# Kernel optimization log

Hardware: AMD Instinct MI355X
Metric: run time of the kernel (lower is better)

## Reference

```python
import jax, jax.numpy as jnp
import numpy as np

DIM = 256
HEADS = 8
G = 8            # group (window) size per axis
POS_DIM = 16     # (dim // 4) // 4
MLP_HIDDEN = 4 * DIM


def layernorm(x, g, b, eps=1e-5):
    m = x.mean(-1, keepdims=True)
    v = ((x - m) ** 2).mean(-1, keepdims=True)
    return (x - m) / jnp.sqrt(v + eps) * g + b


def setup_inputs() -> dict:
    key = jax.random.key(0)
    ks = jax.random.split(key, 32)
    s = 0.02
    d = {}
    d['x'] = jax.random.normal(ks[0], (1, 32768, DIM), jnp.float32)
    d['y'] = jax.random.normal(ks[1], (1, 32768, DIM), jnp.float32)
    d['n1_g'] = jnp.ones((DIM,), jnp.float32)
    d['n1_b'] = jnp.zeros((DIM,), jnp.float32)
    d['qkv_w'] = jax.random.normal(ks[2], (DIM, 3 * DIM), jnp.float32) * s
    d['qkv_b'] = jnp.zeros((3 * DIM,), jnp.float32)
    d['pp_w'] = jax.random.normal(ks[3], (3, POS_DIM), jnp.float32) * s
    d['pp_b'] = jnp.zeros((POS_DIM,), jnp.float32)
    d['p1_lng'] = jnp.ones((POS_DIM,), jnp.float32)
    d['p1_lnb'] = jnp.zeros((POS_DIM,), jnp.float32)
    d['p1_w'] = jax.random.normal(ks[4], (POS_DIM, POS_DIM), jnp.float32) * s
    d['p1_b'] = jnp.zeros((POS_DIM,), jnp.float32)
    d['p2_lng'] = jnp.ones((POS_DIM,), jnp.float32)
    d['p2_lnb'] = jnp.zeros((POS_DIM,), jnp.float32)
    d['p2_w'] = jax.random.normal(ks[5], (POS_DIM, POS_DIM), jnp.float32) * s
    d['p2_b'] = jnp.zeros((POS_DIM,), jnp.float32)
    d['p3_lng'] = jnp.ones((POS_DIM,), jnp.float32)
    d['p3_lnb'] = jnp.zeros((POS_DIM,), jnp.float32)
    d['p3_w'] = jax.random.normal(ks[6], (POS_DIM, HEADS), jnp.float32) * s
    d['p3_b'] = jnp.zeros((HEADS,), jnp.float32)
    d['proj_w'] = jax.random.normal(ks[7], (DIM, DIM), jnp.float32) * s
    d['proj_b'] = jnp.zeros((DIM,), jnp.float32)
    d['n2_g'] = jnp.ones((DIM,), jnp.float32)
    d['n2_b'] = jnp.zeros((DIM,), jnp.float32)
    d['fc1_w'] = jax.random.normal(ks[8], (DIM, MLP_HIDDEN), jnp.float32) * s
    d['fc1_b'] = jnp.zeros((MLP_HIDDEN,), jnp.float32)
    d['fc2_w'] = jax.random.normal(ks[9], (MLP_HIDDEN, DIM), jnp.float32) * s
    d['fc2_b'] = jnp.zeros((DIM,), jnp.float32)
    d['H'] = 32
    d['W'] = 32
    d['D'] = 32
    return d


def reference(x, y, n1_g, n1_b, qkv_w, qkv_b, pp_w, pp_b,
              p1_lng, p1_lnb, p1_w, p1_b, p2_lng, p2_lnb, p2_w, p2_b,
              p3_lng, p3_lnb, p3_w, p3_b, proj_w, proj_b,
              n2_g, n2_b, fc1_w, fc1_b, fc2_w, fc2_b, H, W, D):
    B, L, C = x.shape
    nh, g = HEADS, G
    hd = C // nh
    shortcut = x
    xn = layernorm(x, n1_g, n1_b)
    xv = xn.reshape(B, H, W, D, C)
    yv = y.reshape(B, H, W, D, C)  # note: y is NOT normed in the original

    # SDA window partition (H,W,D divisible by g -> no padding, zero mask)
    def part(t):
        t = t.reshape(B, H // g, g, W // g, g, D // g, g, C)
        t = t.transpose(0, 1, 3, 5, 2, 4, 6, 7)
        return t.reshape(-1, g * g * g, C)

    xg, yg = part(xv), part(yv)
    B_, N, _ = xg.shape

    # original quirk: self.qkv used for BOTH x and y (qkv_y layer unused)
    qkv = (xg @ qkv_w + qkv_b).reshape(B_, N, 3, nh, hd).transpose(2, 0, 3, 1, 4)
    qkv_y = (yg @ qkv_w + qkv_b).reshape(B_, N, 3, nh, hd).transpose(2, 0, 3, 1, 4)
    q = qkv[0] * (hd ** -0.5)
    k_y, v_y = qkv_y[1], qkv_y[2]

    attn = jnp.einsum('bhnd,bhmd->bhnm', q, k_y)  # [B_, nh, N, N]

    # dynamic relative position bias (small MLP + gather)
    rng = jnp.arange(1 - g, g)
    bh, bw, bd = jnp.meshgrid(rng, rng, rng, indexing='ij')
    biases = jnp.stack([bh, bw, bd], -1).reshape(-1, 3).astype(x.dtype)  # [(2g-1)^3, 3]
    pos = biases @ pp_w + pp_b
    pos = jax.nn.relu(layernorm(pos, p1_lng, p1_lnb)) @ p1_w + p1_b
    pos = jax.nn.relu(layernorm(pos, p2_lng, p2_lnb)) @ p2_w + p2_b
    pos = jax.nn.relu(layernorm(pos, p3_lng, p3_lnb)) @ p3_w + p3_b  # [(2g-1)^3, nh]

    c = jnp.arange(g)
    ch, cw, cd = jnp.meshgrid(c, c, c, indexing='ij')
    cf = jnp.stack([ch, cw, cd], 0).reshape(3, -1)          # [3, g^3]
    rel = (cf[:, :, None] - cf[:, None, :]).transpose(1, 2, 0) + (g - 1)
    idx = rel[..., 0] * (2 * g - 1) * (2 * g - 1) + rel[..., 1] * (2 * g - 1) + rel[..., 2]
    bias = pos[idx].transpose(2, 0, 1)  # [nh, N, N]

    attn = jax.nn.softmax(attn + bias[None], axis=-1)
    out = jnp.einsum('bhnm,bhmd->bhnd', attn, v_y).transpose(0, 2, 1, 3).reshape(B_, N, C)
    out = out @ proj_w + proj_b

    # reverse window partition
    out = out.reshape(B, H // g, W // g, D // g, g, g, g, C)
    out = out.transpose(0, 1, 4, 2, 5, 3, 6, 7).reshape(B, H * W * D, C)

    x = shortcut + out
    x2 = layernorm(x, n2_g, n2_b)
    h = jax.nn.gelu(x2 @ fc1_w + fc1_b, approximate=False)
    x = x + (h @ fc2_w + fc2_b)
    return x
```

## Files before the change

kernel.cpp:

```cpp
#include <hip/hip_runtime.h>
#include <cstdint>
#include <cstddef>

typedef unsigned int u32;
typedef unsigned short u16;
typedef __attribute__((ext_vector_type(8))) short bf16x8;
typedef __attribute__((ext_vector_type(4))) float f32x4;

#define DEV __device__ __forceinline__

DEV float b2f(u16 u){ return __uint_as_float(((u32)u)<<16); }
DEV u16 f2b(float f){ u32 x = __float_as_uint(f); x += 0x7fffu + ((x>>16)&1u); return (u16)(x>>16); }
DEV u32 pk2(float a, float b){
  u32 r;
  asm("v_cvt_pk_bf16_f32 %0, %1, %2" : "=v"(r) : "v"(a), "v"(b));
  return r;
}

DEV void gll16(const void* g, void* l){
  __builtin_amdgcn_global_load_lds((const __attribute__((address_space(1))) u32*)g,
                                   (__attribute__((address_space(3))) u32*)l, 16, 0, 0);
}

DEV void win_n(int r, int& win, int& n){
  int d_ = r & 31, w_ = (r>>5)&31, h_ = r>>10;
  win = ((h_>>3)<<4) | ((w_>>3)<<2) | (d_>>3);
  n   = ((h_&7)<<6)  | ((w_&7)<<3)  | (d_&7);
}
DEV int tok_of(int r){
  int win = r>>9, nn = r&511;
  int bh = win>>4, bw=(win>>2)&3, bd=win&3;
  int ih = nn>>6,  iw=(nn>>3)&7,  id=nn&7;
  return ((bh*8+ih)<<10) | ((bw*8+iw)<<5) | (bd*8+id);
}


__global__ void wtrall_k(const float* __restrict__ qkv_w, const float* __restrict__ proj_w,
                         const float* __restrict__ fc1_w, const float* __restrict__ fc2_w,
                         u16* __restrict__ qkvT, u16* __restrict__ projT,
                         u16* __restrict__ fc1T, u16* __restrict__ fc2T){
  int f = blockIdx.x*256 + threadIdx.x;
  const float* w; u16* wt; int g; bool k10 = false; int N;
  if (f < 196608)      { w=qkv_w;  wt=qkvT;  g=f;        N=768;  }
  else if (f < 262144) { w=proj_w; wt=projT; g=f-196608; N=256;  }
  else if (f < 524288) { w=fc1_w;  wt=fc1T;  g=f-262144; N=1024; }
  else                 { w=fc2_w;  wt=fc2T;  g=f-524288; N=256;  k10=true; }
  int n = k10 ? (g>>10) : (g>>8);
  int k = k10 ? (g&1023) : (g&255);
  wt[g] = f2b(w[(size_t)k*N + n]);
}

__global__ void conv_k(const float* __restrict__ x, u16* __restrict__ o, int n4){
  int stride = gridDim.x*blockDim.x;
  for (int i = blockIdx.x*blockDim.x + threadIdx.x; i < n4; i += stride){
    const float4 v = *(const float4*)(x + (size_t)i*4);
    u32 lo = (u32)f2b(v.x) | ((u32)f2b(v.y)<<16);
    u32 hi = (u32)f2b(v.z) | ((u32)f2b(v.w)<<16);
    *(uint2*)(o + (size_t)i*4) = make_uint2(lo, hi);
  }
}

__global__ __launch_bounds__(256)
void ln_k(const float* __restrict__ x, const float* __restrict__ g,
          const float* __restrict__ b, u16* __restrict__ out){
  int row  = blockIdx.x*4 + (threadIdx.x>>6);
  int lane = threadIdx.x & 63;
  const float4 v = *(const float4*)(x + (size_t)row*256 + lane*4);
  float s = v.x+v.y+v.z+v.w;
  #pragma unroll
  for (int m=1;m<64;m<<=1) s += __shfl_xor(s, m);
  float mean = s * (1.0f/256.0f);
  float d0=v.x-mean,d1=v.y-mean,d2=v.z-mean,d3=v.w-mean;
  float q = d0*d0+d1*d1+d2*d2+d3*d3;
  #pragma unroll
  for (int m=1;m<64;m<<=1) q += __shfl_xor(q, m);
  float rs = rsqrtf(q*(1.0f/256.0f) + 1e-5f);
  const float4 gg = *(const float4*)(g + lane*4);
  const float4 bb = *(const float4*)(b + lane*4);
  u32 lo = (u32)f2b(d0*rs*gg.x+bb.x) | ((u32)f2b(d1*rs*gg.y+bb.y)<<16);
  u32 hi = (u32)f2b(d2*rs*gg.z+bb.z) | ((u32)f2b(d3*rs*gg.w+bb.w)<<16);
  *(uint2*)(out + (size_t)row*256 + lane*4) = make_uint2(lo,hi);
}

template<int NOUT>
DEV void pstage(float* v, const float* g, const float* b, const float* W, const float* bb){
  float m = 0.f;
  #pragma unroll
  for (int i=0;i<16;i++) m += v[i];
  m *= 0.0625f;
  float q = 0.f;
  #pragma unroll
  for (int i=0;i<16;i++){ float d=v[i]-m; q += d*d; }
  float rs = rsqrtf(q*0.0625f + 1e-5f);
  float u[16];
  #pragma unroll
  for (int i=0;i<16;i++){ float t = (v[i]-m)*rs*g[i] + b[i]; u[i] = t>0.f?t:0.f; }
  #pragma unroll
  for (int o=0;o<NOUT;o++){
    float s = bb[o];
    #pragma unroll
    for (int kk=0;kk<16;kk++) s += u[kk]*W[kk*NOUT+o];
    v[o] = s;
  }
}

__global__ void posmlp_k(const float* pp_w, const float* pp_b,
                         const float* g1, const float* b1, const float* w1, const float* bb1,
                         const float* g2, const float* b2, const float* w2, const float* bb2,
                         const float* g3, const float* b3, const float* w3, const float* bb3,
                         u16* __restrict__ posb){
  int i = blockIdx.x*256 + threadIdx.x;
  if (i >= 3375) return;
  int t = i;
  int bd = t % 15; t /= 15;
  int bw = t % 15; t /= 15;
  int bh = t;
  float fh = (float)(bh-7), fw = (float)(bw-7), fd = (float)(bd-7);
  float v[16];
  #pragma unroll
  for (int o=0;o<16;o++) v[o] = fh*pp_w[o] + fw*pp_w[16+o] + fd*pp_w[32+o] + pp_b[o];
  pstage<16>(v, g1,b1,w1,bb1);
  pstage<16>(v, g2,b2,w2,bb2);
  pstage<8> (v, g3,b3,w3,bb3);
  #pragma unroll
  for (int h=0;h<8;h++) posb[(size_t)h*3376 + i] = f2b(v[h] * 1.4426950408889634f);
}

struct GemmP {
  const u16* A; const u16* Bt;
  int K;
  const float* bvec;
  float scale;
  const float* add32;
  float* out32;
  u16* out16;
  u16* out16b;
};

template<int MODE>
DEV void epi(const GemmP& p, int r, int c, float val){
  if constexpr (MODE==0){
    float qv = (val + p.bvec[c]) * p.scale;
    int win, n; win_n(r, win, n);
    int hh = c>>5, dd = c&31;
    p.out16[((size_t)((win*8+hh)*512 + n)<<5) + dd] = f2b(qv);
  } else if constexpr (MODE==1){
    float ov = val + p.bvec[c];
    int win, n; win_n(r, win, n);
    int cc = c & 255;
    int hh = cc>>5, dd = cc&31;
    size_t base = (size_t)(win*8+hh)*16384;
    if (c < 256){
      int nc = n>>4, ln2 = ((dd>>3)<<4)|(n&15), jj = dd&7;
      p.out16[base + (size_t)(nc*64+ln2)*8 + jj] = f2b(ov);
    } else {
      int fi = ((n>>5)<<1) | (dd>>4);
      int ln2 = (((n>>3)&3)<<4)|(dd&15), jj = n&7;
      p.out16b[base + (size_t)(fi*64+ln2)*8 + jj] = f2b(ov);
    }
  } else if constexpr (MODE==2){
    int l = tok_of(r);
    size_t o = (size_t)l*256 + c;
    p.out32[o] = val + p.bvec[c] + p.add32[o];
  } else if constexpr (MODE==3){
    float u = val + p.bvec[c];
    float ge = 0.5f*u*(1.0f + erff(u*0.70710678118654752f));
    p.out16[(size_t)r*1024 + c] = f2b(ge);
  } else {
    size_t o = (size_t)r*256 + c;
    p.out32[o] = val + p.bvec[c] + p.add32[o];
  }
}

template<int MODE>
__global__ __launch_bounds__(512)
void gemm256_k(GemmP p){
  __shared__ u16 lA[8][4096];
  __shared__ u16 lB[8][4096];
  const int tid = threadIdx.x;
  const int wid = tid>>6, lane = tid&63;
  const int lr = lane&15, lg = lane>>4;
  const int m0 = blockIdx.y*128, n0 = blockIdx.x*128;
  const int wm = (wid>>2)*64, wn = (wid&3)*32;
  const f32x4 z4 = {0.f,0.f,0.f,0.f};

  #pragma unroll
  for (int it=0; it<8; ++it){
    int off = it*8192 + tid*16;
    int t   = off>>13;
    int row = (off>>6)&127;
    int s   = (off>>4)&3;
    int kc  = s ^ ((row>>1)&3);
    const u16* ga;
    if constexpr (MODE==2){
      int rr = m0+row;
      ga = p.A + ((size_t)((rr>>9)*8 + t)*512 + (rr&511))*32 + kc*8;
    } else {
      ga = p.A + (size_t)(m0+row)*256 + t*32 + kc*8;
    }
    gll16(ga, (char*)lA + off);
    gll16(p.Bt + (size_t)(n0+row)*256 + t*32 + kc*8, (char*)lB + off);
  }
  __syncthreads();

  f32x4 acc[4][2];
  #pragma unroll
  for (int i=0;i<4;i++){ acc[i][0]=z4; acc[i][1]=z4; }

  #pragma unroll
  for (int t=0;t<8;t++){
    bf16x8 af[4], bfr[2];
    #pragma unroll
    for (int i=0;i<4;i++){
      int row = wm + i*16 + lr;
      af[i] = *(const bf16x8*)((const char*)lA + t*8192 + row*64 + ((lg ^ ((row>>1)&3))<<4));
    }
    #pragma unroll
    for (int j=0;j<2;j++){
      int row = wn + j*16 + lr;
      bfr[j] = *(const bf16x8*)((const char*)lB + t*8192 + row*64 + ((lg ^ ((row>>1)&3))<<4));
    }
    #pragma unroll
    for (int i=0;i<4;i++)
      #pragma unroll
      for (int j=0;j<2;j++)
        acc[i][j] = __builtin_amdgcn_mfma_f32_16x16x32_bf16(af[i], bfr[j], acc[i][j], 0,0,0);
  }

  #pragma unroll
  for (int i=0;i<4;i++)
    #pragma unroll
    for (int j=0;j<2;j++)
      #pragma unroll
      for (int v=0;v<4;v++)
        epi<MODE>(p, m0 + wm + i*16 + lg*4 + v, n0 + wn + j*16 + lr, acc[i][j][v]);
}

template<int MODE>
__global__ __launch_bounds__(256)
void gemm_k(GemmP p){
  __shared__ u16 lA[2][4096];
  __shared__ u16 lB[2][4096];
  const int tid = threadIdx.x;
  const int wid = tid>>6, lane = tid&63;
  const int lr = lane&15, lg = lane>>4;
  const int m0 = blockIdx.y*128, n0 = blockIdx.x*128;
  const int K = p.K;
  const int nt = K>>5;
  const int wm = (wid>>1)*64, wn = (wid&1)*64;
  const f32x4 z4 = {0.f,0.f,0.f,0.f};

  f32x4 acc[4][4];
  #pragma unroll
  for (int i=0;i<4;i++)
    #pragma unroll
    for (int j=0;j<4;j++) acc[i][j] = z4;

  #pragma unroll
  for (int r=0;r<2;r++){
    int off = (r*256 + tid)*16;
    int row = off>>6, kc = (off&63)>>1;
    gll16(p.A  + (size_t)(m0+row)*K + kc, (char*)lA[0] + off);
    gll16(p.Bt + (size_t)(n0+row)*K + kc, (char*)lB[0] + off);
  }
  __syncthreads();
  int cur = 0;
  for (int t=0; t<nt; ++t){
    if (t+1 < nt){
      int k0 = (t+1)<<5;
      #pragma unroll
      for (int r=0;r<2;r++){
        int off = (r*256 + tid)*16;
        int row = off>>6, kc = (off&63)>>1;
        gll16(p.A  + (size_t)(m0+row)*K + k0 + kc, (char*)lA[cur^1] + off);
        gll16(p.Bt + (size_t)(n0+row)*K + k0 + kc, (char*)lB[cur^1] + off);
      }
    }
    bf16x8 af[4], bfr[4];
    #pragma unroll
    for (int i=0;i<4;i++){
      af[i]  = *(const bf16x8*)&lA[cur][(wm + i*16 + lr)*32 + lg*8];
      bfr[i] = *(const bf16x8*)&lB[cur][(wn + i*16 + lr)*32 + lg*8];
    }
    #pragma unroll
    for (int i=0;i<4;i++)
      #pragma unroll
      for (int j=0;j<4;j++)
        acc[i][j] = __builtin_amdgcn_mfma_f32_16x16x32_bf16(af[i], bfr[j], acc[i][j], 0,0,0);
    __syncthreads();
    cur ^= 1;
  }

  #pragma unroll
  for (int i=0;i<4;i++)
    #pragma unroll
    for (int j=0;j<4;j++)
      #pragma unroll
      for (int v=0;v<4;v++)
        epi<MODE>(p, m0 + wm + i*16 + lg*4 + v, n0 + wn + j*16 + lr, acc[i][j][v]);
}

__global__ __launch_bounds__(512, 2)
void attn_k(const u16* __restrict__ Q, const u16* __restrict__ Kf,
            const u16* __restrict__ Vf, const u16* __restrict__ posb,
            u16* __restrict__ outF){
  __shared__ u16 lK[16384];
  __shared__ u16 lV[16384];
  __shared__ u16 lP[2][3392];
  const int bid = blockIdx.x;
  const int hh = bid&7;
  const int tid = threadIdx.x, wid = tid>>6, lane = tid&63;
  const int lr = lane&15, lg = lane>>4;
  const u16* Kb = Kf + (size_t)bid*16384;
  const u16* Vb = Vf + (size_t)bid*16384;
  const u16* Qb = Q  + (size_t)bid*16384;
  #pragma unroll
  for (int r=0;r<4;r++){
    int off = (r*512 + tid)*16;
    gll16((const char*)Kb + off, (char*)lK + off);
    gll16((const char*)Vb + off, (char*)lV + off);
  }
  const u16* ptab = posb + (size_t)hh*3376;
  for (int t=tid; t<3375; t+=512){
    u16 u = ptab[t];
    lP[0][t]   = u;
    lP[1][t+1] = u;
  }
  __syncthreads();
  const f32x4 z4 = {0.f,0.f,0.f,0.f};

  for (int ch=0; ch<4; ++ch){
    const int r0 = wid*64 + ch*16;
    const int q  = r0 + lr;
    const int Ab = (q>>6)*225 + ((q>>3)&7)*15 + (q&7) + 1687 - (lg>>1)*15 - (lg&1)*4;
    bf16x8 qf = *(const bf16x8*)(Qb + (size_t)q*32 + lg*8);
    f32x4 o0 = z4, o1 = z4;
    float m = -3.0e38f, s = 0.f;
    #pragma unroll
    for (int ph=0; ph<2; ++ph){
      f32x4 sf[16];
      __builtin_amdgcn_s_setprio(1);
      #pragma unroll
      for (int i=0;i<16;i++){
        int nc = ph*16 + i;
        bf16x8 kf = *(const bf16x8*)&lK[(nc*64 + lane)*8];
        sf[i] = __builtin_amdgcn_mfma_f32_16x16x32_bf16(kf, qf, z4, 0,0,0);
      }
      __builtin_amdgcn_s_setprio(0);
      #pragma unroll
      for (int i=0;i<16;i++){
        int nc = ph*16 + i;
        int idx0 = Ab - (nc>>2)*225 - (nc&3)*30;
        int par = (idx0+1)&1;
        const char* bp = (const char*)lP + ((idx0-3)<<1) + par*6786;
        u32 u1 = *(const u32*)(bp);
        u32 u2 = *(const u32*)(bp + 4);
        sf[i][3] += __uint_as_float(u1<<16);
        sf[i][2] += __uint_as_float(u1 & 0xffff0000u);
        sf[i][1] += __uint_as_float(u2<<16);
        sf[i][0] += __uint_as_float(u2 & 0xffff0000u);
      }
      float pm = -3.0e38f;
      #pragma unroll
      for (int i=0;i<16;i++)
        pm = fmaxf(pm, fmaxf(fmaxf(sf[i][0],sf[i][1]), fmaxf(sf[i][2],sf[i][3])));
      pm = fmaxf(pm, __shfl_xor(pm,16));
      pm = fmaxf(pm, __shfl_xor(pm,32));
      if (ph == 0){
        m = pm;
      } else if (!__all(pm <= m + 8.0f)){
        float mn = fmaxf(m, pm);
        float f = exp2f(m - mn);
        s *= f;
        float f0 = __shfl(f, lg*4+0), f1 = __shfl(f, lg*4+1);
        float f2 = __shfl(f, lg*4+2), f3 = __shfl(f, lg*4+3);
        o0[0]*=f0; o0[1]*=f1; o0[2]*=f2; o0[3]*=f3;
        o1[0]*=f0; o1[1]*=f1; o1[2]*=f2; o1[3]*=f3;
        m = mn;
      }
      float ls = 0.f;
      #pragma unroll
      for (int i=0;i<16;i++){
        #pragma unroll
        for (int v=0;v<4;v++){ float e = exp2f(sf[i][v]-m); sf[i][v]=e; ls+=e; }
      }
      ls += __shfl_xor(ls,16);
      ls += __shfl_xor(ls,32);
      s += ls;
      #pragma unroll
      for (int kc=0;kc<8;kc++){
        u32 a0 = pk2(sf[2*kc  ][0], sf[2*kc  ][1]);
        u32 a1 = pk2(sf[2*kc  ][2], sf[2*kc  ][3]);
        u32 b0 = pk2(sf[2*kc+1][0], sf[2*kc+1][1]);
        u32 b1 = pk2(sf[2*kc+1][2], sf[2*kc+1][3]);
        asm("v_permlane32_swap_b32 %0, %1" : "+v"(a0), "+v"(b0));
        asm("v_permlane16_swap_b32 %0, %1" : "+v"(a0), "+v"(b0));
        asm("v_permlane32_swap_b32 %0, %1" : "+v"(a1), "+v"(b1));
        asm("v_permlane16_swap_b32 %0, %1" : "+v"(a1), "+v"(b1));
        bf16x8 pf;
        ((u32*)&pf)[0]=a0; ((u32*)&pf)[1]=a1; ((u32*)&pf)[2]=b0; ((u32*)&pf)[3]=b1;
        int kcg = ph*8 + kc;
        bf16x8 v0 = *(const bf16x8*)&lV[(size_t)((kcg*2+0)*64 + lane)*8];
        bf16x8 v1 = *(const bf16x8*)&lV[(size_t)((kcg*2+1)*64 + lane)*8];
        __builtin_amdgcn_s_setprio(1);
        o0 = __builtin_amdgcn_mfma_f32_16x16x32_bf16(pf, v0, o0, 0,0,0);
        o1 = __builtin_amdgcn_mfma_f32_16x16x32_bf16(pf, v1, o1, 0,0,0);
        __builtin_amdgcn_s_setprio(0);
      }
    }
    #pragma unroll
    for (int v=0;v<4;v++){
      float inv = 1.0f / __shfl(s, lg*4+v);
      int n = r0 + lg*4 + v;
      size_t base = ((size_t)bid*512 + n)*32;
      outF[base + lr]      = f2b(o0[v]*inv);
      outF[base + 16 + lr] = f2b(o1[v]*inv);
    }
  }
}

extern "C" void kernel_launch(void* const* d_in, const int* in_sizes, int n_in,
                              void* d_out, int out_size, void* d_ws, size_t ws_size,
                              hipStream_t stream){
  const float* x      = (const float*)d_in[0];
  const float* y      = (const float*)d_in[1];
  const float* n1_g   = (const float*)d_in[2];
  const float* n1_b   = (const float*)d_in[3];
  const float* qkv_w  = (const float*)d_in[4];
  const float* qkv_b  = (const float*)d_in[5];
  const float* pp_w   = (const float*)d_in[6];
  const float* pp_b   = (const float*)d_in[7];
  const float* p1_lng = (const float*)d_in[8];
  const float* p1_lnb = (const float*)d_in[9];
  const float* p1_w   = (const float*)d_in[10];
  const float* p1_b   = (const float*)d_in[11];
  const float* p2_lng = (const float*)d_in[12];
  const float* p2_lnb = (const float*)d_in[13];
  const float* p2_w   = (const float*)d_in[14];
  const float* p2_b   = (const float*)d_in[15];
  const float* p3_lng = (const float*)d_in[16];
  const float* p3_lnb = (const float*)d_in[17];
  const float* p3_w   = (const float*)d_in[18];
  const float* p3_b   = (const float*)d_in[19];
  const float* proj_w = (const float*)d_in[20];
  const float* proj_b = (const float*)d_in[21];
  const float* n2_g   = (const float*)d_in[22];
  const float* n2_b   = (const float*)d_in[23];
  const float* fc1_w  = (const float*)d_in[24];
  const float* fc1_b  = (const float*)d_in[25];
  const float* fc2_w  = (const float*)d_in[26];
  const float* fc2_b  = (const float*)d_in[27];
  float* out = (float*)d_out;
  char* ws = (char*)d_ws;

  u16*   qkvT  = (u16*)  (ws + 0);
  u16*   projT = (u16*)  (ws + 393216);
  u16*   fc1T  = (u16*)  (ws + 524288);
  u16*   fc2T  = (u16*)  (ws + 1048576);
  u16*   posb  = (u16*)  (ws + 1572864);
  u16*   xn    = (u16*)  (ws + 5898240);
  u16*   yb    = (u16*)  (ws + 22675456);
  u16*   Qb    = (u16*)  (ws + 39452672);
  u16*   Kfb   = (u16*)  (ws + 56229888);
  u16*   Vfb   = (u16*)  (ws + 73007104);
  u16*   attnF = (u16*)  (ws + 89784320);
  float* xres  = (float*)(ws + 106561536);
  u16*   hbuf  = xn;
  u16*   x2n   = attnF;

  wtrall_k<<<3072,256,0,stream>>>(qkv_w, proj_w, fc1_w, fc2_w, qkvT, projT, fc1T, fc2T);
  posmlp_k<<<14,256,0,stream>>>(pp_w, pp_b,
                                p1_lng,p1_lnb,p1_w,p1_b,
                                p2_lng,p2_lnb,p2_w,p2_b,
                                p3_lng,p3_lnb,p3_w,p3_b, posb);
  ln_k<<<8192,256,0,stream>>>(x, n1_g, n1_b, xn);
  conv_k<<<2048,256,0,stream>>>(y, yb, 2097152);

  GemmP pq; pq.A=xn; pq.Bt=qkvT; pq.K=256; pq.bvec=qkv_b;
  pq.scale=0.17677669529663687f*1.4426950408889634f;
  pq.add32=nullptr; pq.out32=nullptr; pq.out16=Qb; pq.out16b=nullptr;
  gemm256_k<0><<<dim3(2,256),512,0,stream>>>(pq);

  GemmP pkv; pkv.A=yb; pkv.Bt=qkvT + 256*256; pkv.K=256; pkv.bvec=qkv_b + 256;
  pkv.scale=1.f; pkv.add32=nullptr; pkv.out32=nullptr; pkv.out16=Kfb; pkv.out16b=Vfb;
  gemm256_k<1><<<dim3(4,256),512,0,stream>>>(pkv);

  attn_k<<<512,512,0,stream>>>(Qb, Kfb, Vfb, posb, attnF);

  GemmP pp; pp.A=attnF; pp.Bt=projT; pp.K=256; pp.bvec=proj_b;
  pp.scale=1.f; pp.add32=x; pp.out32=xres; pp.out16=nullptr; pp.out16b=nullptr;
  gemm256_k<2><<<dim3(2,256),512,0,stream>>>(pp);

  ln_k<<<8192,256,0,stream>>>(xres, n2_g, n2_b, x2n);

  GemmP pf1; pf1.A=x2n; pf1.Bt=fc1T; pf1.K=256; pf1.bvec=fc1_b;
  pf1.scale=1.f; pf1.add32=nullptr; pf1.out32=nullptr; pf1.out16=hbuf; pf1.out16b=nullptr;
  gemm256_k<3><<<dim3(8,256),512,0,stream>>>(pf1);

  GemmP pf2; pf2.A=hbuf; pf2.Bt=fc2T; pf2.K=1024; pf2.bvec=fc2_b;
  pf2.scale=1.f; pf2.add32=xres; pf2.out32=out; pf2.out16=nullptr; pf2.out16b=nullptr;
  gemm_k<4><<<dim3(2,256),256,0,stream>>>(pf2);
}
```

Measured before the change: 291.6 us.

## Replace full-K 512-thread GEMM with double-buffered GEMM and fp32 position bias table

Removes the gemm256 kernel, which loaded all of K into LDS before computing. All K=256 GEMMs now use the 256-thread double-buffered gemm_k, which gains a MODE 2 attention-layout gather and explicit vmcnt waits plus raw s_barrier in place of __syncthreads. Separately, the relative-position bias table is kept in fp32 and read as floats in attention, replacing the dual-parity bf16 LDS copies. The GEMM change trades a big LDS footprint and one-shot load for a pipelined K loop with smaller 64x64 warp tiles. The bias change doubles table bytes but cuts the unpack arithmetic.

```diff
diff --git a/kernel.cpp b/kernel.cpp
--- a/kernel.cpp
+++ b/kernel.cpp
@@ -108,7 +108,7 @@
                          const float* g1, const float* b1, const float* w1, const float* bb1,
                          const float* g2, const float* b2, const float* w2, const float* bb2,
                          const float* g3, const float* b3, const float* w3, const float* bb3,
-                         u16* __restrict__ posb){
+                         float* __restrict__ posb){
   int i = blockIdx.x*256 + threadIdx.x;
   if (i >= 3375) return;
   int t = i;
@@ -123,7 +123,7 @@
   pstage<16>(v, g2,b2,w2,bb2);
   pstage<8> (v, g3,b3,w3,bb3);
   #pragma unroll
-  for (int h=0;h<8;h++) posb[(size_t)h*3376 + i] = f2b(v[h] * 1.4426950408889634f);
+  for (int h=0;h<8;h++) posb[(size_t)h*3376 + i] = v[h] * 1.4426950408889634f;
 }
 
 struct GemmP {
@@ -173,70 +173,6 @@
 }
 
 template<int MODE>
-__global__ __launch_bounds__(512)
-void gemm256_k(GemmP p){
-  __shared__ u16 lA[8][4096];
-  __shared__ u16 lB[8][4096];
-  const int tid = threadIdx.x;
-  const int wid = tid>>6, lane = tid&63;
-  const int lr = lane&15, lg = lane>>4;
-  const int m0 = blockIdx.y*128, n0 = blockIdx.x*128;
-  const int wm = (wid>>2)*64, wn = (wid&3)*32;
-  const f32x4 z4 = {0.f,0.f,0.f,0.f};
-
-  #pragma unroll
-  for (int it=0; it<8; ++it){
-    int off = it*8192 + tid*16;
-    int t   = off>>13;
-    int row = (off>>6)&127;
-    int s   = (off>>4)&3;
-    int kc  = s ^ ((row>>1)&3);
-    const u16* ga;
-    if constexpr (MODE==2){
-      int rr = m0+row;
-      ga = p.A + ((size_t)((rr>>9)*8 + t)*512 + (rr&511))*32 + kc*8;
-    } else {
-      ga = p.A + (size_t)(m0+row)*256 + t*32 + kc*8;
-    }
-    gll16(ga, (char*)lA + off);
-    gll16(p.Bt + (size_t)(n0+row)*256 + t*32 + kc*8, (char*)lB + off);
-  }
-  __syncthreads();
-
-  f32x4 acc[4][2];
-  #pragma unroll
-  for (int i=0;i<4;i++){ acc[i][0]=z4; acc[i][1]=z4; }
-
-  #pragma unroll
-  for (int t=0;t<8;t++){
-    bf16x8 af[4], bfr[2];
-    #pragma unroll
-    for (int i=0;i<4;i++){
-      int row = wm + i*16 + lr;
-      af[i] = *(const bf16x8*)((const char*)lA + t*8192 + row*64 + ((lg ^ ((row>>1)&3))<<4));
-    }
-    #pragma unroll
-    for (int j=0;j<2;j++){
-      int row = wn + j*16 + lr;
-      bfr[j] = *(const bf16x8*)((const char*)lB + t*8192 + row*64 + ((lg ^ ((row>>1)&3))<<4));
-    }
-    #pragma unroll
-    for (int i=0;i<4;i++)
-      #pragma unroll
-      for (int j=0;j<2;j++)
-        acc[i][j] = __builtin_amdgcn_mfma_f32_16x16x32_bf16(af[i], bfr[j], acc[i][j], 0,0,0);
-  }
-
-  #pragma unroll
-  for (int i=0;i<4;i++)
-    #pragma unroll
-    for (int j=0;j<2;j++)
-      #pragma unroll
-      for (int v=0;v<4;v++)
-        epi<MODE>(p, m0 + wm + i*16 + lg*4 + v, n0 + wn + j*16 + lr, acc[i][j][v]);
-}
-
-template<int MODE>
 __global__ __launch_bounds__(256)
 void gemm_k(GemmP p){
   __shared__ u16 lA[2][4096];
@@ -250,32 +186,41 @@
   const int wm = (wid>>1)*64, wn = (wid&1)*64;
   const f32x4 z4 = {0.f,0.f,0.f,0.f};
 
+  auto stage = [&](int buf, int t){
+    #pragma unroll
+    for (int r=0;r<2;r++){
+      int off = (r*256 + tid)*16;
+      int row = off>>6, kc = (off&63)>>1;
+      int kcol = (t<<5) + kc;
+      const u16* ga;
+      if constexpr (MODE==2){
+        int rr = m0 + row;
+        ga = p.A + ((size_t)((rr>>9)*8 + (kcol>>5))*512 + (rr&511))*32 + (kcol&31);
+      } else {
+        ga = p.A + (size_t)(m0+row)*K + kcol;
+      }
+      gll16(ga, (char*)lA[buf] + off);
+      gll16(p.Bt + (size_t)(n0+row)*K + kcol, (char*)lB[buf] + off);
+    }
+  };
+
   f32x4 acc[4][4];
   #pragma unroll
   for (int i=0;i<4;i++)
     #pragma unroll
     for (int j=0;j<4;j++) acc[i][j] = z4;
 
-  #pragma unroll
-  for (int r=0;r<2;r++){
-    int off = (r*256 + tid)*16;
-    int row = off>>6, kc = (off&63)>>1;
-    gll16(p.A  + (size_t)(m0+row)*K + kc, (char*)lA[0] + off);
-    gll16(p.Bt + (size_t)(n0+row)*K + kc, (char*)lB[0] + off);
-  }
-  __syncthreads();
+  stage(0, 0);
   int cur = 0;
   for (int t=0; t<nt; ++t){
     if (t+1 < nt){
-      int k0 = (t+1)<<5;
-      #pragma unroll
-      for (int r=0;r<2;r++){
-        int off = (r*256 + tid)*16;
-        int row = off>>6, kc = (off&63)>>1;
-        gll16(p.A  + (size_t)(m0+row)*K + k0 + kc, (char*)lA[cur^1] + off);
-        gll16(p.Bt + (size_t)(n0+row)*K + k0 + kc, (char*)lB[cur^1] + off);
-      }
-    }
+      stage(cur^1, t+1);
+      asm volatile("s_waitcnt vmcnt(4)" ::: "memory");
+    } else {
+      asm volatile("s_waitcnt vmcnt(0)" ::: "memory");
+    }
+    __builtin_amdgcn_s_barrier();
+    __builtin_amdgcn_sched_barrier(0);
     bf16x8 af[4], bfr[4];
     #pragma unroll
     for (int i=0;i<4;i++){
@@ -287,7 +232,10 @@
       #pragma unroll
       for (int j=0;j<4;j++)
         acc[i][j] = __builtin_amdgcn_mfma_f32_16x16x32_bf16(af[i], bfr[j], acc[i][j], 0,0,0);
-    __syncthreads();
+    if (t+1 < nt){
+      __builtin_amdgcn_sched_barrier(0);
+      __builtin_amdgcn_s_barrier();
+    }
     cur ^= 1;
   }
 
@@ -302,11 +250,11 @@
 
 __global__ __launch_bounds__(512, 2)
 void attn_k(const u16* __restrict__ Q, const u16* __restrict__ Kf,
-            const u16* __restrict__ Vf, const u16* __restrict__ posb,
+            const u16* __restrict__ Vf, const float* __restrict__ posb,
             u16* __restrict__ outF){
   __shared__ u16 lK[16384];
   __shared__ u16 lV[16384];
-  __shared__ u16 lP[2][3392];
+  __shared__ float lPf[3392];
   const int bid = blockIdx.x;
   const int hh = bid&7;
   const int tid = threadIdx.x, wid = tid>>6, lane = tid&63;
@@ -320,12 +268,8 @@
     gll16((const char*)Kb + off, (char*)lK + off);
     gll16((const char*)Vb + off, (char*)lV + off);
   }
-  const u16* ptab = posb + (size_t)hh*3376;
-  for (int t=tid; t<3375; t+=512){
-    u16 u = ptab[t];
-    lP[0][t]   = u;
-    lP[1][t+1] = u;
-  }
+  const float* ptab = posb + (size_t)hh*3376;
+  for (int t=tid; t<3375; t+=512) lPf[t] = ptab[t];
   __syncthreads();
   const f32x4 z4 = {0.f,0.f,0.f,0.f};
 
@@ -350,15 +294,11 @@
       #pragma unroll
       for (int i=0;i<16;i++){
         int nc = ph*16 + i;
-        int idx0 = Ab - (nc>>2)*225 - (nc&3)*30;
-        int par = (idx0+1)&1;
-        const char* bp = (const char*)lP + ((idx0-3)<<1) + par*6786;
-        u32 u1 = *(const u32*)(bp);
-        u32 u2 = *(const u32*)(bp + 4);
-        sf[i][3] += __uint_as_float(u1<<16);
-        sf[i][2] += __uint_as_float(u1 & 0xffff0000u);
-        sf[i][1] += __uint_as_float(u2<<16);
-        sf[i][0] += __uint_as_float(u2 & 0xffff0000u);
+        const float* bp = lPf + (Ab - (nc>>2)*225 - (nc&3)*30 - 3);
+        sf[i][3] += bp[0];
+        sf[i][2] += bp[1];
+        sf[i][1] += bp[2];
+        sf[i][0] += bp[3];
       }
       float pm = -3.0e38f;
       #pragma unroll
@@ -457,7 +397,7 @@
   u16*   projT = (u16*)  (ws + 393216);
   u16*   fc1T  = (u16*)  (ws + 524288);
   u16*   fc2T  = (u16*)  (ws + 1048576);
-  u16*   posb  = (u16*)  (ws + 1572864);
+  float* posb  = (float*)(ws + 1572864);
   u16*   xn    = (u16*)  (ws + 5898240);
   u16*   yb    = (u16*)  (ws + 22675456);
   u16*   Qb    = (u16*)  (ws + 39452672);
@@ -479,23 +419,23 @@
   GemmP pq; pq.A=xn; pq.Bt=qkvT; pq.K=256; pq.bvec=qkv_b;
   pq.scale=0.17677669529663687f*1.4426950408889634f;
   pq.add32=nullptr; pq.out32=nullptr; pq.out16=Qb; pq.out16b=nullptr;
-  gemm256_k<0><<<dim3(2,256),512,0,stream>>>(pq);
+  gemm_k<0><<<dim3(2,256),256,0,stream>>>(pq);
 
   GemmP pkv; pkv.A=yb; pkv.Bt=qkvT + 256*256; pkv.K=256; pkv.bvec=qkv_b + 256;
   pkv.scale=1.f; pkv.add32=nullptr; pkv.out32=nullptr; pkv.out16=Kfb; pkv.out16b=Vfb;
-  gemm256_k<1><<<dim3(4,256),512,0,stream>>>(pkv);
+  gemm_k<1><<<dim3(4,256),256,0,stream>>>(pkv);
 
   attn_k<<<512,512,0,stream>>>(Qb, Kfb, Vfb, posb, attnF);
 
   GemmP pp; pp.A=attnF; pp.Bt=projT; pp.K=256; pp.bvec=proj_b;
   pp.scale=1.f; pp.add32=x; pp.out32=xres; pp.out16=nullptr; pp.out16b=nullptr;
-  gemm256_k<2><<<dim3(2,256),512,0,stream>>>(pp);
+  gemm_k<2><<<dim3(2,256),256,0,stream>>>(pp);
 
   ln_k<<<8192,256,0,stream>>>(xres, n2_g, n2_b, x2n);
 
   GemmP pf1; pf1.A=x2n; pf1.Bt=fc1T; pf1.K=256; pf1.bvec=fc1_b;
   pf1.scale=1.f; pf1.add32=nullptr; pf1.out32=nullptr; pf1.out16=hbuf; pf1.out16b=nullptr;
-  gemm256_k<3><<<dim3(8,256),512,0,stream>>>(pf1);
+  gemm_k<3><<<dim3(8,256),256,0,stream>>>(pf1);
 
   GemmP pf2; pf2.A=hbuf; pf2.Bt=fc2T; pf2.K=1024; pf2.bvec=fc2_b;
   pf2.scale=1.f; pf2.add32=xres; pf2.out32=out; pf2.out16=nullptr; pf2.out16b=nullptr;
```

After: 282.4 us. 1.03x faster.
